# Kernel optimization log

Hardware: AMD Instinct MI355X
Metric: run time of the kernel (lower is better)

## Reference

```python
import jax, jax.numpy as jnp
import numpy as np

N = 8192  # number of nodes


def _deg_norm(idx, n):
    # degree^{-1/2}, zero-degree clamped to 1 (DGL allow_zero_in_degree behavior)
    deg = jax.ops.segment_sum(jnp.ones(idx.shape[0], jnp.float32), idx, num_segments=n)
    return jax.lax.rsqrt(jnp.maximum(deg, 1.0))


def _graph_conv(h, src, dst, norm_src, norm_dst, W, b):
    # norm='both': scale at src, sparse sum-aggregate, scale at dst, then linear
    h = h * norm_src[:, None]
    m = jax.ops.segment_sum(h[src], dst, num_segments=h.shape[0])  # gather + scatter-add
    m = m * norm_dst[:, None]
    return m @ W + b


def setup_inputs() -> dict:
    key = jax.random.key(0)
    k = jax.random.split(key, 6)
    E = 262144
    x = jax.random.normal(k[0], (N, 256), jnp.float32)
    src = jax.random.randint(k[1], (E,), 0, N, jnp.int32)
    dst = jax.random.randint(k[2], (E,), 0, N, jnp.int32)
    W1 = jax.random.normal(k[3], (256, 128), jnp.float32) * (1.0 / np.sqrt(256))
    b1 = jnp.zeros((128,), jnp.float32)
    W2 = jax.random.normal(k[4], (128, 128), jnp.float32) * (1.0 / np.sqrt(128))
    b2 = jnp.zeros((128,), jnp.float32)
    return {"x": x, "src": src, "dst": dst, "W1": W1, "b1": b1, "W2": W2, "b2": b2}


def reference(x, src, dst, W1, b1, W2, b2):
    n = x.shape[0]
    norm_src = _deg_norm(src, n)  # out-degree norm
    norm_dst = _deg_norm(dst, n)  # in-degree norm
    # encode: GraphConv -> relu -> GraphConv  (dropout=0 -> identity)
    h = jax.nn.relu(_graph_conv(x, src, dst, norm_src, norm_dst, W1, b1))
    h = _graph_conv(h, src, dst, norm_src, norm_dst, W2, b2)
    # decode: sigmoid(h h^T), dense [N, N] reconstruction
    return jax.nn.sigmoid(h @ h.T)
```

## Files before the change

### kernel.cpp

```cpp
#include <hip/hip_runtime.h>
#include <hip/hip_bf16.h>

typedef __attribute__((ext_vector_type(8))) short short8;
typedef __attribute__((ext_vector_type(4))) float f32x4;

#define NNODES 8192
#define FDIM 128

__global__ void k_zero(int* __restrict__ p, int n) {
    int i = blockIdx.x * blockDim.x + threadIdx.x;
    if (i < n) p[i] = 0;
}

__global__ void k_deg_int(const int* __restrict__ src, const int* __restrict__ dst,
                          int* __restrict__ cnt_s, int* __restrict__ cnt_d, int E) {
    int e = blockIdx.x * blockDim.x + threadIdx.x;
    if (e < E) {
        atomicAdd(&cnt_s[src[e]], 1);
        atomicAdd(&cnt_d[dst[e]], 1);
    }
}

__global__ __launch_bounds__(256) void k_scan_norms(const int* __restrict__ cnt_s,
                                                    const int* __restrict__ cnt_d,
                                                    float* __restrict__ norm_s,
                                                    float* __restrict__ norm_d,
                                                    int* __restrict__ row_start,
                                                    int* __restrict__ cursor, int n) {
    __shared__ int partial[256];
    __shared__ int offs[257];
    int t = threadIdx.x;
    int base = t * 32;
#pragma unroll
    for (int i = 0; i < 32; ++i) {
        norm_s[base + i] = rsqrtf(fmaxf((float)cnt_s[base + i], 1.0f));
        norm_d[base + i] = rsqrtf(fmaxf((float)cnt_d[base + i], 1.0f));
    }
    int local[32];
    int s = 0;
#pragma unroll
    for (int i = 0; i < 32; ++i) { local[i] = s; s += cnt_d[base + i]; }
    partial[t] = s;
    __syncthreads();
    if (t == 0) {
        int acc = 0;
        for (int i = 0; i < 256; ++i) { offs[i] = acc; acc += partial[i]; }
        offs[256] = acc;
    }
    __syncthreads();
    int o = offs[t];
#pragma unroll
    for (int i = 0; i < 32; ++i) {
        int v = o + local[i];
        row_start[base + i] = v;
        cursor[base + i] = v;
    }
    if (t == 0) row_start[n] = offs[256];
}

__global__ void k_fill(const int* __restrict__ src, const int* __restrict__ dst,
                       int* __restrict__ cursor, int* __restrict__ csr_src, int E) {
    int e = blockIdx.x * blockDim.x + threadIdx.x;
    if (e < E) {
        int pos = atomicAdd(&cursor[dst[e]], 1);
        csr_src[pos] = src[e];
    }
}

template<int K>
__global__ __launch_bounds__(256) void k_linear(const float* __restrict__ X,
                                                const float* __restrict__ W,
                                                const float* __restrict__ norm,
                                                float* __restrict__ Y) {
    __shared__ float xs[16][K];
    int t = threadIdx.x;
    int row0 = blockIdx.x * 16;
    constexpr int K4 = K / 4;
    constexpr int NCH = 16 * K4 / 256;
#pragma unroll
    for (int i = 0; i < NCH; ++i) {
        int c = t + i * 256;
        int r = c / K4, k4 = c % K4;
        *(float4*)&xs[r][k4 * 4] = *(const float4*)(X + (size_t)(row0 + r) * K + k4 * 4);
    }
    __syncthreads();

    int lane = t & 31, g = t >> 5;
    int r0 = g * 2, r1 = g * 2 + 1;
    int c = lane * 4;
    f32x4 acc0 = {0.f, 0.f, 0.f, 0.f}, acc1 = {0.f, 0.f, 0.f, 0.f};
    for (int k = 0; k < K; k += 4) {
        f32x4 x0 = *(f32x4*)&xs[r0][k];
        f32x4 x1 = *(f32x4*)&xs[r1][k];
#pragma unroll
        for (int kk = 0; kk < 4; ++kk) {
            f32x4 w = *(const f32x4*)(W + (size_t)(k + kk) * FDIM + c);
            acc0 += w * x0[kk];
            acc1 += w * x1[kk];
        }
    }
    float n0 = norm[row0 + r0], n1 = norm[row0 + r1];
    *(f32x4*)(Y + (size_t)(row0 + r0) * FDIM + c) = acc0 * n0;
    *(f32x4*)(Y + (size_t)(row0 + r1) * FDIM + c) = acc1 * n1;
}

static __device__ inline unsigned short f2bf(float f) {
    union { float f; unsigned int u; } a; a.f = f;
    unsigned int u = a.u;
    unsigned int r = u + 0x7FFFu + ((u >> 16) & 1u);
    return (unsigned short)(r >> 16);
}

template<int MODE>
__global__ __launch_bounds__(256) void k_gather_agg(const float* __restrict__ Y,
                                                    const int* __restrict__ row_start,
                                                    const int* __restrict__ csr_src,
                                                    const float* __restrict__ nd,
                                                    const float* __restrict__ bias,
                                                    void* __restrict__ outp) {
    int t = threadIdx.x;
    int node = blockIdx.x * 8 + (t >> 5);
    int c4 = (t & 31) << 2;
    int beg = row_start[node], end = row_start[node + 1];
    f32x4 acc = {0.f, 0.f, 0.f, 0.f};
    int e = beg;
    for (; e + 1 < end; e += 2) {
        int s0 = csr_src[e], s1 = csr_src[e + 1];
        f32x4 v0 = *(const f32x4*)(Y + ((size_t)s0 << 7) + c4);
        f32x4 v1 = *(const f32x4*)(Y + ((size_t)s1 << 7) + c4);
        acc += v0;
        acc += v1;
    }
    if (e < end) {
        int s0 = csr_src[e];
        acc += *(const f32x4*)(Y + ((size_t)s0 << 7) + c4);
    }
    float scale = nd[node];
    f32x4 b = *(const f32x4*)(bias + c4);
    f32x4 v = acc * scale + b;
    if (MODE == 0) {
#pragma unroll
        for (int i = 0; i < 4; ++i) v[i] = fmaxf(v[i], 0.f);
        *(f32x4*)((float*)outp + ((size_t)node << 7) + c4) = v;
    } else {
        ushort4 u;
        u.x = f2bf(v[0]); u.y = f2bf(v[1]); u.z = f2bf(v[2]); u.w = f2bf(v[3]);
        *(ushort4*)((unsigned short*)outp + ((size_t)node << 7) + c4) = u;
    }
}

__global__ __launch_bounds__(256) void k_decode(const __hip_bfloat16* __restrict__ H,
                                                float* __restrict__ C) {
    __shared__ __align__(16) unsigned char smem[65536];
    unsigned char* sA = smem;
    unsigned char* sB = smem + 32768;
    const int ti = blockIdx.x, tj = blockIdx.y;
    const int t = threadIdx.x;
    const unsigned char* gH = (const unsigned char*)H;

#pragma unroll
    for (int i = 0; i < 8; ++i) {
        int chunk = t + i * 256;
        int row = chunk >> 4;
        int cc = (chunk & 15) << 4;
        int lofs = row * 256 + (cc ^ ((row & 7) << 4));
        *(float4*)(sA + lofs) = *(const float4*)(gH + ((size_t)(ti * 128 + row) << 8) + cc);
        *(float4*)(sB + lofs) = *(const float4*)(gH + ((size_t)(tj * 128 + row) << 8) + cc);
    }
    __syncthreads();

    const int w = t >> 6, lane = t & 63;
    const int wr = (w >> 1) * 64, wc = (w & 1) * 64;
    const int lr = lane & 15;
    const int lk = (lane >> 4) * 16;

    f32x4 acc[4][4] = {};

#pragma unroll
    for (int ks = 0; ks < 4; ++ks) {
        short8 af[4], bfr[4];
#pragma unroll
        for (int mi = 0; mi < 4; ++mi) {
            int row = wr + mi * 16 + lr;
            int off = row * 256 + ((ks * 64 + lk) ^ ((row & 7) << 4));
            af[mi] = *(const short8*)(sA + off);
        }
#pragma unroll
        for (int ni = 0; ni < 4; ++ni) {
            int row = wc + ni * 16 + lr;
            int off = row * 256 + ((ks * 64 + lk) ^ ((row & 7) << 4));
            bfr[ni] = *(const short8*)(sB + off);
        }
#pragma unroll
        for (int mi = 0; mi < 4; ++mi)
#pragma unroll
            for (int ni = 0; ni < 4; ++ni)
                acc[mi][ni] = __builtin_amdgcn_mfma_f32_16x16x32_bf16(af[mi], bfr[ni],
                                                                      acc[mi][ni], 0, 0, 0);
    }

    const int rbase = (lane >> 4) * 4;
    const int cbase = lane & 15;
#pragma unroll
    for (int mi = 0; mi < 4; ++mi) {
#pragma unroll
        for (int ni = 0; ni < 4; ++ni) {
#pragma unroll
            for (int r = 0; r < 4; ++r) {
                int row = ti * 128 + wr + mi * 16 + rbase + r;
                int col = tj * 128 + wc + ni * 16 + cbase;
                float v = acc[mi][ni][r];
                C[(size_t)row * NNODES + col] = 1.0f / (1.0f + __expf(-v));
            }
        }
    }
}

extern "C" void kernel_launch(void* const* d_in, const int* in_sizes, int n_in,
                              void* d_out, int out_size, void* d_ws, size_t ws_size,
                              hipStream_t stream) {
    const float* x  = (const float*)d_in[0];
    const int* src  = (const int*)d_in[1];
    const int* dst  = (const int*)d_in[2];
    const float* W1 = (const float*)d_in[3];
    const float* b1 = (const float*)d_in[4];
    const float* W2 = (const float*)d_in[5];
    const float* b2 = (const float*)d_in[6];
    float* out = (float*)d_out;
    const int E = in_sizes[1];

    char* ws = (char*)d_ws;
    float* norm_s    = (float*)(ws + 0);
    float* norm_d    = (float*)(ws + (32 << 10));
    int*   cnt_s     = (int*)(ws + (64 << 10));
    int*   cnt_d     = (int*)(ws + (96 << 10));
    int*   row_start = (int*)(ws + (128 << 10));
    int*   cursor    = (int*)(ws + (164 << 10));
    int*   csr_src   = (int*)(ws + (196 << 10));
    char*  big       = ws + (196 << 10) + ((size_t)E * 4);
    float* bufA      = (float*)big;
    float* bufB      = (float*)(big + (4 << 20));
    __hip_bfloat16* h2bf = (__hip_bfloat16*)(big + (8 << 20));

    k_zero<<<(2 * NNODES + 255) / 256, 256, 0, stream>>>(cnt_s, 2 * NNODES);

    k_deg_int<<<(E + 255) / 256, 256, 0, stream>>>(src, dst, cnt_s, cnt_d, E);
    k_scan_norms<<<1, 256, 0, stream>>>(cnt_s, cnt_d, norm_s, norm_d, row_start, cursor, NNODES);
    k_fill<<<(E + 255) / 256, 256, 0, stream>>>(src, dst, cursor, csr_src, E);

    k_linear<256><<<NNODES / 16, 256, 0, stream>>>(x, W1, norm_s, bufA);
    k_gather_agg<0><<<NNODES / 8, 256, 0, stream>>>(bufA, row_start, csr_src, norm_d, b1, bufB);

    k_linear<128><<<NNODES / 16, 256, 0, stream>>>(bufB, W2, norm_s, bufA);
    k_gather_agg<1><<<NNODES / 8, 256, 0, stream>>>(bufA, row_start, csr_src, norm_d, b2, h2bf);

    k_decode<<<dim3(64, 64), 256, 0, stream>>>(h2bf, out);
}
```

Baseline: 189.9 us.

## Exploit symmetry of H·Hᵀ in decode and unroll gather aggregation

The decode kernel now skips blocks below the diagonal. Each upper-triangle tile computes its sigmoid once and writes it to both (i,j) and (j,i) with nontemporal stores, which halves the MFMA and LDS-load work over the 64x64 grid. The gather-aggregate loop is unrolled to four edges with two independent accumulators to expose more memory-level parallelism. The in-degree norm is derived from the CSR row_start difference instead of a separate norm_d array, which removes a buffer and its load. The cost is that half of the decode blocks exit idle and the mirrored stores use a different access pattern, so total output write traffic is unchanged.

Result: slower. 211.9 us (+11.6%).

```diff
diff --git a/kernel.cpp b/kernel.cpp
--- a/kernel.cpp
+++ b/kernel.cpp
@@ -24,7 +24,6 @@
 __global__ __launch_bounds__(256) void k_scan_norms(const int* __restrict__ cnt_s,
                                                     const int* __restrict__ cnt_d,
                                                     float* __restrict__ norm_s,
-                                                    float* __restrict__ norm_d,
                                                     int* __restrict__ row_start,
                                                     int* __restrict__ cursor, int n) {
     __shared__ int partial[256];
@@ -32,10 +31,8 @@
     int t = threadIdx.x;
     int base = t * 32;
 #pragma unroll
-    for (int i = 0; i < 32; ++i) {
+    for (int i = 0; i < 32; ++i)
         norm_s[base + i] = rsqrtf(fmaxf((float)cnt_s[base + i], 1.0f));
-        norm_d[base + i] = rsqrtf(fmaxf((float)cnt_d[base + i], 1.0f));
-    }
     int local[32];
     int s = 0;
 #pragma unroll
@@ -115,27 +112,28 @@
 __global__ __launch_bounds__(256) void k_gather_agg(const float* __restrict__ Y,
                                                     const int* __restrict__ row_start,
                                                     const int* __restrict__ csr_src,
-                                                    const float* __restrict__ nd,
                                                     const float* __restrict__ bias,
                                                     void* __restrict__ outp) {
     int t = threadIdx.x;
     int node = blockIdx.x * 8 + (t >> 5);
     int c4 = (t & 31) << 2;
     int beg = row_start[node], end = row_start[node + 1];
-    f32x4 acc = {0.f, 0.f, 0.f, 0.f};
+    f32x4 acc0 = {0.f, 0.f, 0.f, 0.f}, acc1 = {0.f, 0.f, 0.f, 0.f};
     int e = beg;
-    for (; e + 1 < end; e += 2) {
-        int s0 = csr_src[e], s1 = csr_src[e + 1];
+    for (; e + 3 < end; e += 4) {
+        int s0 = csr_src[e], s1 = csr_src[e + 1], s2 = csr_src[e + 2], s3 = csr_src[e + 3];
         f32x4 v0 = *(const f32x4*)(Y + ((size_t)s0 << 7) + c4);
         f32x4 v1 = *(const f32x4*)(Y + ((size_t)s1 << 7) + c4);
-        acc += v0;
-        acc += v1;
-    }
-    if (e < end) {
+        f32x4 v2 = *(const f32x4*)(Y + ((size_t)s2 << 7) + c4);
+        f32x4 v3 = *(const f32x4*)(Y + ((size_t)s3 << 7) + c4);
+        acc0 += v0; acc1 += v1; acc0 += v2; acc1 += v3;
+    }
+    for (; e < end; ++e) {
         int s0 = csr_src[e];
-        acc += *(const f32x4*)(Y + ((size_t)s0 << 7) + c4);
-    }
-    float scale = nd[node];
+        acc0 += *(const f32x4*)(Y + ((size_t)s0 << 7) + c4);
+    }
+    f32x4 acc = acc0 + acc1;
+    float scale = rsqrtf(fmaxf((float)(end - beg), 1.0f));
     f32x4 b = *(const f32x4*)(bias + c4);
     f32x4 v = acc * scale + b;
     if (MODE == 0) {
@@ -151,10 +149,11 @@
 
 __global__ __launch_bounds__(256) void k_decode(const __hip_bfloat16* __restrict__ H,
                                                 float* __restrict__ C) {
+    const int ti = blockIdx.x, tj = blockIdx.y;
+    if (tj < ti) return;
     __shared__ __align__(16) unsigned char smem[65536];
     unsigned char* sA = smem;
     unsigned char* sB = smem + 32768;
-    const int ti = blockIdx.x, tj = blockIdx.y;
     const int t = threadIdx.x;
     const unsigned char* gH = (const unsigned char*)H;
 
@@ -203,14 +202,19 @@
     const int cbase = lane & 15;
 #pragma unroll
     for (int mi = 0; mi < 4; ++mi) {
+        int rowb = ti * 128 + wr + mi * 16 + rbase;
 #pragma unroll
         for (int ni = 0; ni < 4; ++ni) {
-#pragma unroll
-            for (int r = 0; r < 4; ++r) {
-                int row = ti * 128 + wr + mi * 16 + rbase + r;
-                int col = tj * 128 + wc + ni * 16 + cbase;
-                float v = acc[mi][ni][r];
-                C[(size_t)row * NNODES + col] = 1.0f / (1.0f + __expf(-v));
+            int col = tj * 128 + wc + ni * 16 + cbase;
+            f32x4 s;
+#pragma unroll
+            for (int r = 0; r < 4; ++r)
+                s[r] = 1.0f / (1.0f + __expf(-acc[mi][ni][r]));
+            __builtin_nontemporal_store(s, (f32x4*)(C + (size_t)col * NNODES + rowb));
+            if (ti != tj) {
+#pragma unroll
+                for (int r = 0; r < 4; ++r)
+                    __builtin_nontemporal_store(s[r], C + (size_t)(rowb + r) * NNODES + col);
             }
         }
     }
@@ -231,7 +235,6 @@
 
     char* ws = (char*)d_ws;
     float* norm_s    = (float*)(ws + 0);
-    float* norm_d    = (float*)(ws + (32 << 10));
     int*   cnt_s     = (int*)(ws + (64 << 10));
     int*   cnt_d     = (int*)(ws + (96 << 10));
     int*   row_start = (int*)(ws + (128 << 10));
@@ -245,14 +248,14 @@
     k_zero<<<(2 * NNODES + 255) / 256, 256, 0, stream>>>(cnt_s, 2 * NNODES);
 
     k_deg_int<<<(E + 255) / 256, 256, 0, stream>>>(src, dst, cnt_s, cnt_d, E);
-    k_scan_norms<<<1, 256, 0, stream>>>(cnt_s, cnt_d, norm_s, norm_d, row_start, cursor, NNODES);
+    k_scan_norms<<<1, 256, 0, stream>>>(cnt_s, cnt_d, norm_s, row_start, cursor, NNODES);
     k_fill<<<(E + 255) / 256, 256, 0, stream>>>(src, dst, cursor, csr_src, E);
 
     k_linear<256><<<NNODES / 16, 256, 0, stream>>>(x, W1, norm_s, bufA);
-    k_gather_agg<0><<<NNODES / 8, 256, 0, stream>>>(bufA, row_start, csr_src, norm_d, b1, bufB);
+    k_gather_agg<0><<<NNODES / 8, 256, 0, stream>>>(bufA, row_start, csr_src, b1, bufB);
 
     k_linear<128><<<NNODES / 16, 256, 0, stream>>>(bufB, W2, norm_s, bufA);
-    k_gather_agg<1><<<NNODES / 8, 256, 0, stream>>>(bufA, row_start, csr_src, norm_d, b2, h2bf);
+    k_gather_agg<1><<<NNODES / 8, 256, 0, stream>>>(bufA, row_start, csr_src, b2, h2bf);
 
     k_decode<<<dim3(64, 64), 256, 0, stream>>>(h2bf, out);
 }
```

## Store projected features in bf16 for gathers and use nontemporal decode stores

Applied to the files above, without the earlier changes.

The linear layers now write their projected node features as bf16 instead of fp32. The gather-aggregate kernels read these 8-wide bf16 vectors, accumulate in fp32, use 16 nodes per block, and compute the destination norm from the CSR row length, so the norm_d buffer is gone. This halves gather traffic on the random-access aggregation. The decode epilogue uses a fast reciprocal and nontemporal stores for the large dense output, which lowers its write cost but adds bf16 rounding error in the intermediate features.

Result: slower. 223.1 us (+17.5%).

```diff
diff --git a/kernel.cpp b/kernel.cpp
--- a/kernel.cpp
+++ b/kernel.cpp
@@ -6,6 +6,17 @@
 
 #define NNODES 8192
 #define FDIM 128
+
+static __device__ inline unsigned short f2bf(float f) {
+    union { float f; unsigned int u; } a; a.f = f;
+    unsigned int u = a.u;
+    unsigned int r = u + 0x7FFFu + ((u >> 16) & 1u);
+    return (unsigned short)(r >> 16);
+}
+
+static __device__ inline float bf2f(unsigned short u) {
+    union { unsigned int u; float f; } c; c.u = ((unsigned int)u) << 16; return c.f;
+}
 
 __global__ void k_zero(int* __restrict__ p, int n) {
     int i = blockIdx.x * blockDim.x + threadIdx.x;
@@ -24,7 +35,6 @@
 __global__ __launch_bounds__(256) void k_scan_norms(const int* __restrict__ cnt_s,
                                                     const int* __restrict__ cnt_d,
                                                     float* __restrict__ norm_s,
-                                                    float* __restrict__ norm_d,
                                                     int* __restrict__ row_start,
                                                     int* __restrict__ cursor, int n) {
     __shared__ int partial[256];
@@ -32,10 +42,8 @@
     int t = threadIdx.x;
     int base = t * 32;
 #pragma unroll
-    for (int i = 0; i < 32; ++i) {
+    for (int i = 0; i < 32; ++i)
         norm_s[base + i] = rsqrtf(fmaxf((float)cnt_s[base + i], 1.0f));
-        norm_d[base + i] = rsqrtf(fmaxf((float)cnt_d[base + i], 1.0f));
-    }
     int local[32];
     int s = 0;
 #pragma unroll
@@ -71,7 +79,7 @@
 __global__ __launch_bounds__(256) void k_linear(const float* __restrict__ X,
                                                 const float* __restrict__ W,
                                                 const float* __restrict__ norm,
-                                                float* __restrict__ Y) {
+                                                unsigned short* __restrict__ Y) {
     __shared__ float xs[16][K];
     int t = threadIdx.x;
     int row0 = blockIdx.x * 16;
@@ -100,52 +108,68 @@
         }
     }
     float n0 = norm[row0 + r0], n1 = norm[row0 + r1];
-    *(f32x4*)(Y + (size_t)(row0 + r0) * FDIM + c) = acc0 * n0;
-    *(f32x4*)(Y + (size_t)(row0 + r1) * FDIM + c) = acc1 * n1;
-}
-
-static __device__ inline unsigned short f2bf(float f) {
-    union { float f; unsigned int u; } a; a.f = f;
-    unsigned int u = a.u;
-    unsigned int r = u + 0x7FFFu + ((u >> 16) & 1u);
-    return (unsigned short)(r >> 16);
+    acc0 *= n0; acc1 *= n1;
+    ushort4 u0, u1;
+    u0.x = f2bf(acc0[0]); u0.y = f2bf(acc0[1]); u0.z = f2bf(acc0[2]); u0.w = f2bf(acc0[3]);
+    u1.x = f2bf(acc1[0]); u1.y = f2bf(acc1[1]); u1.z = f2bf(acc1[2]); u1.w = f2bf(acc1[3]);
+    *(ushort4*)(Y + (size_t)(row0 + r0) * FDIM + c) = u0;
+    *(ushort4*)(Y + (size_t)(row0 + r1) * FDIM + c) = u1;
 }
 
 template<int MODE>
-__global__ __launch_bounds__(256) void k_gather_agg(const float* __restrict__ Y,
+__global__ __launch_bounds__(256) void k_gather_agg(const unsigned short* __restrict__ Y,
                                                     const int* __restrict__ row_start,
                                                     const int* __restrict__ csr_src,
-                                                    const float* __restrict__ nd,
                                                     const float* __restrict__ bias,
                                                     void* __restrict__ outp) {
     int t = threadIdx.x;
-    int node = blockIdx.x * 8 + (t >> 5);
-    int c4 = (t & 31) << 2;
+    int node = blockIdx.x * 16 + (t >> 4);
+    int c8 = (t & 15) << 3;
     int beg = row_start[node], end = row_start[node + 1];
-    f32x4 acc = {0.f, 0.f, 0.f, 0.f};
+    f32x4 a0 = {0.f, 0.f, 0.f, 0.f}, a1 = {0.f, 0.f, 0.f, 0.f};
+    f32x4 b0 = {0.f, 0.f, 0.f, 0.f}, b1 = {0.f, 0.f, 0.f, 0.f};
     int e = beg;
     for (; e + 1 < end; e += 2) {
         int s0 = csr_src[e], s1 = csr_src[e + 1];
-        f32x4 v0 = *(const f32x4*)(Y + ((size_t)s0 << 7) + c4);
-        f32x4 v1 = *(const f32x4*)(Y + ((size_t)s1 << 7) + c4);
-        acc += v0;
-        acc += v1;
+        short8 v0 = *(const short8*)(Y + ((size_t)s0 << 7) + c8);
+        short8 v1 = *(const short8*)(Y + ((size_t)s1 << 7) + c8);
+#pragma unroll
+        for (int i = 0; i < 4; ++i) {
+            a0[i] += bf2f((unsigned short)v0[i]);
+            a1[i] += bf2f((unsigned short)v0[i + 4]);
+            b0[i] += bf2f((unsigned short)v1[i]);
+            b1[i] += bf2f((unsigned short)v1[i + 4]);
+        }
     }
     if (e < end) {
         int s0 = csr_src[e];
-        acc += *(const f32x4*)(Y + ((size_t)s0 << 7) + c4);
-    }
-    float scale = nd[node];
-    f32x4 b = *(const f32x4*)(bias + c4);
-    f32x4 v = acc * scale + b;
+        short8 v0 = *(const short8*)(Y + ((size_t)s0 << 7) + c8);
+#pragma unroll
+        for (int i = 0; i < 4; ++i) {
+            a0[i] += bf2f((unsigned short)v0[i]);
+            a1[i] += bf2f((unsigned short)v0[i + 4]);
+        }
+    }
+    a0 += b0; a1 += b1;
+    float scale = rsqrtf(fmaxf((float)(end - beg), 1.0f));
+    f32x4 bb0 = *(const f32x4*)(bias + c8);
+    f32x4 bb1 = *(const f32x4*)(bias + c8 + 4);
+    f32x4 v0 = a0 * scale + bb0;
+    f32x4 v1 = a1 * scale + bb1;
     if (MODE == 0) {
 #pragma unroll
-        for (int i = 0; i < 4; ++i) v[i] = fmaxf(v[i], 0.f);
-        *(f32x4*)((float*)outp + ((size_t)node << 7) + c4) = v;
+        for (int i = 0; i < 4; ++i) { v0[i] = fmaxf(v0[i], 0.f); v1[i] = fmaxf(v1[i], 0.f); }
+        float* o = (float*)outp + ((size_t)node << 7) + c8;
+        *(f32x4*)o = v0;
+        *(f32x4*)(o + 4) = v1;
     } else {
-        ushort4 u;
-        u.x = f2bf(v[0]); u.y = f2bf(v[1]); u.z = f2bf(v[2]); u.w = f2bf(v[3]);
-        *(ushort4*)((unsigned short*)outp + ((size_t)node << 7) + c4) = u;
+        short8 u;
+#pragma unroll
+        for (int i = 0; i < 4; ++i) {
+            u[i] = (short)f2bf(v0[i]);
+            u[i + 4] = (short)f2bf(v1[i]);
+        }
+        *(short8*)((unsigned short*)outp + ((size_t)node << 7) + c8) = u;
     }
 }
 
@@ -203,14 +227,14 @@
     const int cbase = lane & 15;
 #pragma unroll
     for (int mi = 0; mi < 4; ++mi) {
+        int rowb = ti * 128 + wr + mi * 16 + rbase;
 #pragma unroll
         for (int ni = 0; ni < 4; ++ni) {
+            int col = tj * 128 + wc + ni * 16 + cbase;
 #pragma unroll
             for (int r = 0; r < 4; ++r) {
-                int row = ti * 128 + wr + mi * 16 + rbase + r;
-                int col = tj * 128 + wc + ni * 16 + cbase;
-                float v = acc[mi][ni][r];
-                C[(size_t)row * NNODES + col] = 1.0f / (1.0f + __expf(-v));
+                float s = __builtin_amdgcn_rcpf(1.0f + __expf(-acc[mi][ni][r]));
+                __builtin_nontemporal_store(s, C + (size_t)(rowb + r) * NNODES + col);
             }
         }
     }
@@ -231,28 +255,27 @@
 
     char* ws = (char*)d_ws;
     float* norm_s    = (float*)(ws + 0);
-    float* norm_d    = (float*)(ws + (32 << 10));
     int*   cnt_s     = (int*)(ws + (64 << 10));
     int*   cnt_d     = (int*)(ws + (96 << 10));
     int*   row_start = (int*)(ws + (128 << 10));
     int*   cursor    = (int*)(ws + (164 << 10));
     int*   csr_src   = (int*)(ws + (196 << 10));
     char*  big       = ws + (196 << 10) + ((size_t)E * 4);
-    float* bufA      = (float*)big;
-    float* bufB      = (float*)(big + (4 << 20));
-    __hip_bfloat16* h2bf = (__hip_bfloat16*)(big + (8 << 20));
+    unsigned short* ybf  = (unsigned short*)big;
+    float*          h1   = (float*)(big + (2 << 20));
+    __hip_bfloat16* h2bf = (__hip_bfloat16*)(big + (6 << 20));
 
     k_zero<<<(2 * NNODES + 255) / 256, 256, 0, stream>>>(cnt_s, 2 * NNODES);
 
     k_deg_int<<<(E + 255) / 256, 256, 0, stream>>>(src, dst, cnt_s, cnt_d, E);
-    k_scan_norms<<<1, 256, 0, stream>>>(cnt_s, cnt_d, norm_s, norm_d, row_start, cursor, NNODES);
+    k_scan_norms<<<1, 256, 0, stream>>>(cnt_s, cnt_d, norm_s, row_start, cursor, NNODES);
     k_fill<<<(E + 255) / 256, 256, 0, stream>>>(src, dst, cursor, csr_src, E);
 
-    k_linear<256><<<NNODES / 16, 256, 0, stream>>>(x, W1, norm_s, bufA);
-    k_gather_agg<0><<<NNODES / 8, 256, 0, stream>>>(bufA, row_start, csr_src, norm_d, b1, bufB);
-
-    k_linear<128><<<NNODES / 16, 256, 0, stream>>>(bufB, W2, norm_s, bufA);
-    k_gather_agg<1><<<NNODES / 8, 256, 0, stream>>>(bufA, row_start, csr_src, norm_d, b2, h2bf);
+    k_linear<256><<<NNODES / 16, 256, 0, stream>>>(x, W1, norm_s, ybf);
+    k_gather_agg<0><<<NNODES / 16, 256, 0, stream>>>(ybf, row_start, csr_src, b1, h1);
+
+    k_linear<128><<<NNODES / 16, 256, 0, stream>>>(h1, W2, norm_s, ybf);
+    k_gather_agg<1><<<NNODES / 16, 256, 0, stream>>>(ybf, row_start, csr_src, b2, h2bf);
 
     k_decode<<<dim3(64, 64), 256, 0, stream>>>(h2bf, out);
 }
```
